# Performance work log

Hardware: AMD Instinct MI355X
Metric: run time of the kernel (lower is better)

The kernel has to match this reference:

```python
import jax, jax.numpy as jnp
import numpy as np

D_MODEL = 1024
NUM_HEADS = 16
HEAD_DIM = D_MODEL // NUM_HEADS


def setup_inputs() -> dict:
    key = jax.random.key(0)
    ks = jax.random.split(key, 9)
    s = D_MODEL ** -0.5  # roughly like nn.Linear init scale
    x = jax.random.normal(ks[0], (4, 2048, D_MODEL), dtype=jnp.float32)
    Wq = jax.random.normal(ks[1], (D_MODEL, D_MODEL), dtype=jnp.float32) * s
    bq = jax.random.normal(ks[2], (D_MODEL,), dtype=jnp.float32) * s
    Wk = jax.random.normal(ks[3], (D_MODEL, D_MODEL), dtype=jnp.float32) * s
    bk = jax.random.normal(ks[4], (D_MODEL,), dtype=jnp.float32) * s
    Wv = jax.random.normal(ks[5], (D_MODEL, D_MODEL), dtype=jnp.float32) * s
    bv = jax.random.normal(ks[6], (D_MODEL,), dtype=jnp.float32) * s
    Wo = jax.random.normal(ks[7], (D_MODEL, D_MODEL), dtype=jnp.float32) * s
    bo = jax.random.normal(ks[8], (D_MODEL,), dtype=jnp.float32) * s
    return {"x": x, "Wq": Wq, "bq": bq, "Wk": Wk, "bk": bk,
            "Wv": Wv, "bv": bv, "Wo": Wo, "bo": bo}


def reference(x, Wq, bq, Wk, bk, Wv, bv, Wo, bo):
    B, S, D = x.shape
    H, Dh = NUM_HEADS, HEAD_DIM
    scale = Dh ** -0.5
    # nn.Linear: x @ W.T + b
    q = (x @ Wq.T + bq).reshape(B, S, H, Dh)
    k = (x @ Wk.T + bk).reshape(B, S, H, Dh)
    v = (x @ Wv.T + bv).reshape(B, S, H, Dh)
    # scores: (B, H, S, S), full materialization as in the original bmm path
    dp = scale * jnp.einsum('bqhd,bkhd->bhqk', q, k)
    att = jax.nn.softmax(dp, axis=-1)
    out = jnp.einsum('bhqk,bkhd->bqhd', att, v).reshape(B, S, D)
    return out @ Wo.T + bo
```

## Files before the change

kernel.cpp:

```cpp
#include <hip/hip_runtime.h>
#include <stdint.h>

typedef __attribute__((ext_vector_type(8))) __bf16 bf16x8;
typedef __attribute__((ext_vector_type(4))) float floatx4;

#define DEV __device__ __forceinline__

DEV unsigned short f2bf(float f) {
    union { float f; unsigned u; } uf; uf.f = f;
    unsigned u = uf.u;
    unsigned r = (u + 0x7fffu + ((u >> 16) & 1u)) >> 16;
    return (unsigned short)r;
}

DEV float fast_exp2(float x) {
#if __has_builtin(__builtin_amdgcn_exp2f)
    return __builtin_amdgcn_exp2f(x);
#else
    return exp2f(x);
#endif
}

DEV unsigned pack_trunc2(float lo, float hi) {
    return __builtin_amdgcn_perm(__float_as_uint(hi), __float_as_uint(lo), 0x07060302u);
}

DEV void async16(const void* g, void* l) {
    __builtin_amdgcn_global_load_lds(
        (const __attribute__((address_space(1))) void*)g,
        (__attribute__((address_space(3))) void*)l, 16, 0, 0);
}

__global__ void cast_bf16_kernel(const float* __restrict__ src,
                                 unsigned short* __restrict__ dst, int n4) {
    int i = blockIdx.x * blockDim.x + threadIdx.x;
    if (i >= n4) return;
    float4 v = reinterpret_cast<const float4*>(src)[i];
    ushort4 o;
    o.x = f2bf(v.x); o.y = f2bf(v.y); o.z = f2bf(v.z); o.w = f2bf(v.w);
    reinterpret_cast<ushort4*>(dst)[i] = o;
}

__global__ void cast_w_kernel(const float* __restrict__ Wq, const float* __restrict__ Wk,
                              const float* __restrict__ Wv, const float* __restrict__ Wo,
                              const float* __restrict__ bq, const float* __restrict__ bk,
                              const float* __restrict__ bv,
                              unsigned short* __restrict__ wqkv,
                              unsigned short* __restrict__ wo,
                              float* __restrict__ bqkv) {
    const int NW = 262144;
    int i = blockIdx.x * blockDim.x + threadIdx.x;
    if (i < 4 * NW) {
        int seg = i >> 18, off = i & (NW - 1);
        const float* src = (seg == 0) ? Wq : (seg == 1) ? Wk : (seg == 2) ? Wv : Wo;
        unsigned short* dst = (seg < 3) ? (wqkv + seg * 1048576) : wo;
        float4 v = reinterpret_cast<const float4*>(src)[off];
        ushort4 o;
        o.x = f2bf(v.x); o.y = f2bf(v.y); o.z = f2bf(v.z); o.w = f2bf(v.w);
        reinterpret_cast<ushort4*>(dst)[off] = o;
    } else {
        int j = i - 4 * NW;
        if (j < 768) {
            int seg = j >> 8, off = j & 255;
            const float* src = (seg == 0) ? bq : (seg == 1) ? bk : bv;
            reinterpret_cast<float4*>(bqkv)[j] =
                reinterpret_cast<const float4*>(src)[off];
        }
    }
}

template <int MODE>
__global__ __launch_bounds__(256)
void gemm128(const unsigned short* __restrict__ A,
             const unsigned short* __restrict__ B,
             const float* __restrict__ bias,
             unsigned short* __restrict__ q_ws,
             unsigned short* __restrict__ k_ws,
             unsigned short* __restrict__ v_ws,
             float* __restrict__ fout) {
    constexpr int K = 1024;
    __shared__ alignas(16) unsigned short smem[128 * 136];
    unsigned short* sA = smem;
    unsigned short* sB = smem + 128 * 64;
    unsigned short* sT = smem;
    float* sT32 = reinterpret_cast<float*>(smem);

    const int tid = threadIdx.x;
    const int w = tid >> 6, lane = tid & 63, quad = lane >> 4, l16 = lane & 15;
    const int wr = w >> 1, wc = w & 1;
    const int bm = blockIdx.x, bn = blockIdx.y;
    const int arow0 = bm * 128, brow0 = bn * 128;

    floatx4 acc[4][4];
#pragma unroll
    for (int i = 0; i < 4; i++)
#pragma unroll
        for (int j = 0; j < 4; j++) acc[i][j] = (floatx4){0.f, 0.f, 0.f, 0.f};

    for (int k0 = 0; k0 < K; k0 += 64) {
#pragma unroll
        for (int i = 0; i < 4; i++) {
            int cb = i * 256 + w * 64;
            int ci = cb + lane;
            int row = ci >> 3, cl = ci & 7, cs = cl ^ (row & 7);
            async16(A + (size_t)(arow0 + row) * K + k0 + cs * 8, (char*)sA + cb * 16);
            async16(B + (size_t)(brow0 + row) * K + k0 + cs * 8, (char*)sB + cb * 16);
        }
        __syncthreads();
#pragma unroll
        for (int kk = 0; kk < 2; kk++) {
            bf16x8 aF[4], bF[4];
#pragma unroll
            for (int i = 0; i < 4; i++) {
                int row = wr * 64 + i * 16 + l16;
                int c = kk * 4 + quad, ph = c ^ (row & 7);
                aF[i] = *reinterpret_cast<const bf16x8*>(sA + row * 64 + ph * 8);
            }
#pragma unroll
            for (int j = 0; j < 4; j++) {
                int row = wc * 64 + j * 16 + l16;
                int c = kk * 4 + quad, ph = c ^ (row & 7);
                bF[j] = *reinterpret_cast<const bf16x8*>(sB + row * 64 + ph * 8);
            }
#pragma unroll
            for (int i = 0; i < 4; i++)
#pragma unroll
                for (int j = 0; j < 4; j++)
                    acc[i][j] = __builtin_amdgcn_mfma_f32_16x16x32_bf16(
                        aF[i], bF[j], acc[i][j], 0, 0, 0);
        }
        __syncthreads();
    }

    if (MODE == 1) {
#pragma unroll
        for (int ch = 0; ch < 2; ch++) {
            if (ch) __syncthreads();
            if (wr == ch) {
#pragma unroll
                for (int j = 0; j < 4; j++) {
                    const int c = wc * 64 + j * 16 + l16;
                    const float bia = bias[brow0 + c];
#pragma unroll
                    for (int i = 0; i < 4; i++) {
                        int s_loc = i * 16 + quad * 4;
#pragma unroll
                        for (int r = 0; r < 4; r++)
                            sT32[(s_loc + r) * 132 + c] = acc[i][j][r] + bia;
                    }
                }
            }
            __syncthreads();
            const int cpos = (tid & 31) * 4;
#pragma unroll
            for (int it = 0; it < 8; it++) {
                int s_loc = (tid >> 5) + it * 8;
                int grow = arow0 + ch * 64 + s_loc;
                float4 vv = *reinterpret_cast<const float4*>(sT32 + s_loc * 132 + cpos);
                *reinterpret_cast<float4*>(fout + (size_t)grow * 1024 + brow0 + cpos) = vv;
            }
        }
    } else if (bn < 16) {
        unsigned short* dst = (bn < 8) ? q_ws : k_ws;
        const float sc = (bn < 8) ? 0.18033688f : 1.0f;
#pragma unroll
        for (int j = 0; j < 4; j++) {
            const int c = wc * 64 + j * 16 + l16;
            const float bia = bias[brow0 + c];
#pragma unroll
            for (int i = 0; i < 4; i++) {
                int s_loc = wr * 64 + i * 16 + quad * 4;
#pragma unroll
                for (int r = 0; r < 4; r++)
                    sT[(s_loc + r) * 136 + c] = f2bf((acc[i][j][r] + bia) * sc);
            }
        }
        __syncthreads();
        const int nnbase = (bn & 7) * 128;
        const int c0 = (tid & 15) * 8;
        const int h = (nnbase + c0) >> 6, d = c0 & 63;
#pragma unroll
        for (int it = 0; it < 8; it++) {
            int s_loc = (tid >> 4) + it * 16;
            int s = arow0 + s_loc;
            int bb = s >> 11, s4 = s & 2047;
            uint4 vdat = *reinterpret_cast<const uint4*>(sT + s_loc * 136 + c0);
            *reinterpret_cast<uint4*>(
                dst + ((size_t)(bb * 16 + h) * 2048 + s4) * 64 + d) = vdat;
        }
    } else {
#pragma unroll
        for (int j = 0; j < 4; j++) {
            const int c = wc * 64 + j * 16 + l16;
            const float bia = bias[brow0 + c];
#pragma unroll
            for (int i = 0; i < 4; i++) {
                int v_hi = wr * 4 + i;
#pragma unroll
                for (int r = 0; r < 4; r++) {
                    int v = (quad * 4 + r) * 8 + v_hi;
                    sT[c * 136 + v] = f2bf(acc[i][j][r] + bia);
                }
            }
        }
        __syncthreads();
        const int bb = bm >> 4, blk = bm & 15;
        const int chunk = tid & 15;
#pragma unroll
        for (int it = 0; it < 8; it++) {
            int row = (tid >> 4) + it * 16;
            int h = (bn - 16) * 2 + (row >> 6), d = row & 63;
            ushort4 lo = *reinterpret_cast<const ushort4*>(sT + row * 136 + chunk * 8);
            ushort4 hi = *reinterpret_cast<const ushort4*>(sT + row * 136 + chunk * 8 + 4);
            size_t off = ((size_t)(bb * 16 + h) * 64 + d) * 2048 + blk * 128 + chunk * 8;
            *reinterpret_cast<ushort4*>(v_ws + off) = lo;
            *reinterpret_cast<ushort4*>(v_ws + off + 4) = hi;
        }
    }
}

__global__ __launch_bounds__(256, 5)
void attn_kernel(const unsigned short* __restrict__ q_ws,
                 const unsigned short* __restrict__ k_ws,
                 const unsigned short* __restrict__ v_ws,
                 unsigned short* __restrict__ o_ws) {
    __shared__ alignas(16) unsigned short smem[2 * 128 * 64];
    unsigned short* sK  = smem;
    unsigned short* sVt = smem + 128 * 64;

    const int tid = threadIdx.x;
    const int w = tid >> 6, lane = tid & 63, quad = lane >> 4, l16 = lane & 15;
    const int id = blockIdx.x;
    const int bh = (id >> 8) * 8 + (id & 7);
    const int q0 = ((id >> 3) & 31) * 64;
    const size_t base = (size_t)bh * 2048 * 64;

    unsigned short* sPw = smem + w * 2048;

    bf16x8 aQ[2];
    {
        int qrow = q0 + w * 16 + l16;
        const unsigned short* qp = q_ws + base + (size_t)qrow * 64 + quad * 8;
        aQ[0] = *reinterpret_cast<const bf16x8*>(qp);
        aQ[1] = *reinterpret_cast<const bf16x8*>(qp + 32);
    }

    const unsigned short* kptr[4];
    const unsigned short* vptr[4];
    char* klds[4];
    char* vlds[4];
#pragma unroll
    for (int i = 0; i < 4; i++) {
        int cb = i * 256 + w * 64;
        int ci = cb + lane;
        {
            int row = ci >> 3, cl = ci & 7, cs = cl ^ (row & 7);
            kptr[i] = k_ws + base + (size_t)row * 64 + cs * 8;
            klds[i] = (char*)sK + cb * 16;
        }
        {
            int row = ci >> 4, cl = ci & 15, cs = cl ^ (row & 15);
            vptr[i] = v_ws + base + (size_t)row * 2048 + cs * 8;
            vlds[i] = (char*)sVt + cb * 16;
        }
    }

    const __bf16 one = (__bf16)1.0f;
    const bf16x8 vOnes = {one, one, one, one, one, one, one, one};

    floatx4 oAcc[4], rsAcc;
#pragma unroll
    for (int j = 0; j < 4; j++) oAcc[j] = (floatx4){0.f, 0.f, 0.f, 0.f};
    rsAcc = (floatx4){0.f, 0.f, 0.f, 0.f};

    for (int t = 0; t < 16; t++) {
        const int kv0 = t * 128;
#pragma unroll
        for (int i = 0; i < 4; i++) {
            async16(kptr[i] + (size_t)kv0 * 64, klds[i]);
            async16(vptr[i] + kv0, vlds[i]);
        }
        __syncthreads();

        floatx4 sAcc[8];
#pragma unroll
        for (int j = 0; j < 8; j++) sAcc[j] = (floatx4){0.f, 0.f, 0.f, 0.f};
#pragma unroll
        for (int kk = 0; kk < 2; kk++) {
#pragma unroll
            for (int j = 0; j < 8; j++) {
                int krow = j * 16 + l16;
                int c = kk * 4 + quad, ph = c ^ (krow & 7);
                bf16x8 bK = *reinterpret_cast<const bf16x8*>(sK + krow * 64 + ph * 8);
                sAcc[j] = __builtin_amdgcn_mfma_f32_16x16x32_bf16(aQ[kk], bK, sAcc[j], 0, 0, 0);
            }
        }

        uint4 pk[4];
#pragma unroll
        for (int r = 0; r < 4; r++) {
            float e[8];
#pragma unroll
            for (int j = 0; j < 8; j++) e[j] = fast_exp2(sAcc[j][r]);
            pk[r].x = pack_trunc2(e[0], e[1]);
            pk[r].y = pack_trunc2(e[2], e[3]);
            pk[r].z = pack_trunc2(e[4], e[5]);
            pk[r].w = pack_trunc2(e[6], e[7]);
        }
        __syncthreads();

#pragma unroll
        for (int r = 0; r < 4; r++) {
            int row = quad * 4 + r;
            *reinterpret_cast<uint4*>(sPw + row * 128 + ((l16 ^ row) & 15) * 8) = pk[r];
        }
        asm volatile("s_waitcnt lgkmcnt(0)" ::: "memory");

        bf16x8 aP[4];
#pragma unroll
        for (int ks = 0; ks < 4; ks++)
            aP[ks] = *reinterpret_cast<const bf16x8*>(
                sPw + l16 * 128 + (((ks * 4 + quad) ^ l16) & 15) * 8);
#pragma unroll
        for (int jd = 0; jd < 4; jd++) {
            int drow = jd * 16 + l16;
#pragma unroll
            for (int ks = 0; ks < 4; ks++) {
                int c = ks * 4 + quad, ph = c ^ (drow & 15);
                bf16x8 bV = *reinterpret_cast<const bf16x8*>(sVt + drow * 128 + ph * 8);
                oAcc[jd] = __builtin_amdgcn_mfma_f32_16x16x32_bf16(aP[ks], bV, oAcc[jd], 0, 0, 0);
            }
        }
#pragma unroll
        for (int ks = 0; ks < 4; ks++)
            rsAcc = __builtin_amdgcn_mfma_f32_16x16x32_bf16(aP[ks], vOnes, rsAcc, 0, 0, 0);
        __syncthreads();
    }

    float inv[4];
#pragma unroll
    for (int r = 0; r < 4; r++) inv[r] = 1.0f / rsAcc[r];
    const int bb = bh >> 4, h = bh & 15;
#pragma unroll
    for (int jd = 0; jd < 4; jd++) {
        int d = jd * 16 + l16;
#pragma unroll
        for (int r = 0; r < 4; r++) {
            int s = q0 + w * 16 + quad * 4 + r;
            float v = oAcc[jd][r] * inv[r];
            o_ws[((size_t)bb * 2048 + s) * 1024 + h * 64 + d] = f2bf(v);
        }
    }
}

extern "C" void kernel_launch(void* const* d_in, const int* in_sizes, int n_in,
                              void* d_out, int out_size, void* d_ws, size_t ws_size,
                              hipStream_t stream) {
    const float* x  = (const float*)d_in[0];
    const float* Wq = (const float*)d_in[1];
    const float* bq = (const float*)d_in[2];
    const float* Wk = (const float*)d_in[3];
    const float* bk = (const float*)d_in[4];
    const float* Wv = (const float*)d_in[5];
    const float* bv = (const float*)d_in[6];
    const float* Wo = (const float*)d_in[7];
    const float* bo = (const float*)d_in[8];
    float* out = (float*)d_out;

    char* ws = (char*)d_ws;
    unsigned short* xb   = (unsigned short*)(ws);
    unsigned short* wqkv = (unsigned short*)(ws + (16ull << 20));
    unsigned short* wo   = (unsigned short*)(ws + (22ull << 20));
    float*          bqkv = (float*)(ws + (24ull << 20));
    unsigned short* q_ws = (unsigned short*)(ws + (25ull << 20));
    unsigned short* k_ws = (unsigned short*)(ws + (41ull << 20));
    unsigned short* v_ws = (unsigned short*)(ws + (57ull << 20));
    unsigned short* o_ws = xb;

    const int n4x = 8192 * 1024 / 4;
    cast_bf16_kernel<<<n4x / 256, 256, 0, stream>>>(x, xb, n4x);
    cast_w_kernel<<<4099, 256, 0, stream>>>(Wq, Wk, Wv, Wo, bq, bk, bv,
                                            wqkv, wo, bqkv);

    gemm128<0><<<dim3(64, 24), 256, 0, stream>>>(xb, wqkv, bqkv, q_ws, k_ws, v_ws, nullptr);
    attn_kernel<<<2048, 256, 0, stream>>>(q_ws, k_ws, v_ws, o_ws);
    gemm128<1><<<dim3(64, 8), 256, 0, stream>>>(o_ws, wo, bo, nullptr, nullptr, nullptr, out);
}
```

Baseline: 288.3 us.

## Double-buffer K/V tiles in attention and merge cast kernels

The attention kernel now walks the sequence in 64-key tiles and prefetches the next K/V tile into a second LDS buffer while computing on the current one. This leaves one barrier per iteration instead of three and lets global loads overlap with MFMA work. The x and weight cast kernels are merged into a single launch, and the V-transpose staging index in the QKV GEMM is remapped. The risk is higher LDS use and a lower occupancy hint (4 instead of 5), plus more loop iterations with smaller tiles.

```diff
diff --git a/kernel.cpp b/kernel.cpp
--- a/kernel.cpp
+++ b/kernel.cpp
@@ -31,41 +31,41 @@
         (__attribute__((address_space(3))) void*)l, 16, 0, 0);
 }
 
-__global__ void cast_bf16_kernel(const float* __restrict__ src,
-                                 unsigned short* __restrict__ dst, int n4) {
-    int i = blockIdx.x * blockDim.x + threadIdx.x;
-    if (i >= n4) return;
-    float4 v = reinterpret_cast<const float4*>(src)[i];
-    ushort4 o;
-    o.x = f2bf(v.x); o.y = f2bf(v.y); o.z = f2bf(v.z); o.w = f2bf(v.w);
-    reinterpret_cast<ushort4*>(dst)[i] = o;
-}
-
-__global__ void cast_w_kernel(const float* __restrict__ Wq, const float* __restrict__ Wk,
-                              const float* __restrict__ Wv, const float* __restrict__ Wo,
-                              const float* __restrict__ bq, const float* __restrict__ bk,
-                              const float* __restrict__ bv,
-                              unsigned short* __restrict__ wqkv,
-                              unsigned short* __restrict__ wo,
-                              float* __restrict__ bqkv) {
+__global__ void cast_all_kernel(const float* __restrict__ x,
+                                const float* __restrict__ Wq, const float* __restrict__ Wk,
+                                const float* __restrict__ Wv, const float* __restrict__ Wo,
+                                const float* __restrict__ bq, const float* __restrict__ bk,
+                                const float* __restrict__ bv,
+                                unsigned short* __restrict__ xb,
+                                unsigned short* __restrict__ wqkv,
+                                unsigned short* __restrict__ wo,
+                                float* __restrict__ bqkv) {
+    const int NX = 2097152;
     const int NW = 262144;
     int i = blockIdx.x * blockDim.x + threadIdx.x;
-    if (i < 4 * NW) {
-        int seg = i >> 18, off = i & (NW - 1);
+    if (i < NX) {
+        float4 v = reinterpret_cast<const float4*>(x)[i];
+        ushort4 o;
+        o.x = f2bf(v.x); o.y = f2bf(v.y); o.z = f2bf(v.z); o.w = f2bf(v.w);
+        reinterpret_cast<ushort4*>(xb)[i] = o;
+        return;
+    }
+    int j = i - NX;
+    if (j < 4 * NW) {
+        int seg = j >> 18, off = j & (NW - 1);
         const float* src = (seg == 0) ? Wq : (seg == 1) ? Wk : (seg == 2) ? Wv : Wo;
         unsigned short* dst = (seg < 3) ? (wqkv + seg * 1048576) : wo;
         float4 v = reinterpret_cast<const float4*>(src)[off];
         ushort4 o;
         o.x = f2bf(v.x); o.y = f2bf(v.y); o.z = f2bf(v.z); o.w = f2bf(v.w);
         reinterpret_cast<ushort4*>(dst)[off] = o;
-    } else {
-        int j = i - 4 * NW;
-        if (j < 768) {
-            int seg = j >> 8, off = j & 255;
-            const float* src = (seg == 0) ? bq : (seg == 1) ? bk : bv;
-            reinterpret_cast<float4*>(bqkv)[j] =
-                reinterpret_cast<const float4*>(src)[off];
-        }
+        return;
+    }
+    int k = j - 4 * NW;
+    if (k < 768) {
+        int seg = k >> 8, off = k & 255;
+        const float* src = (seg == 0) ? bq : (seg == 1) ? bk : bv;
+        reinterpret_cast<float4*>(bqkv)[k] = reinterpret_cast<const float4*>(src)[off];
     }
 }
 
@@ -195,10 +195,9 @@
             const float bia = bias[brow0 + c];
 #pragma unroll
             for (int i = 0; i < 4; i++) {
-                int v_hi = wr * 4 + i;
 #pragma unroll
                 for (int r = 0; r < 4; r++) {
-                    int v = (quad * 4 + r) * 8 + v_hi;
+                    int v = wr * 64 + (quad * 4 + r) * 4 + i;
                     sT[c * 136 + v] = f2bf(acc[i][j][r] + bia);
                 }
             }
@@ -219,14 +218,12 @@
     }
 }
 
-__global__ __launch_bounds__(256, 5)
+__global__ __launch_bounds__(256, 4)
 void attn_kernel(const unsigned short* __restrict__ q_ws,
                  const unsigned short* __restrict__ k_ws,
                  const unsigned short* __restrict__ v_ws,
                  unsigned short* __restrict__ o_ws) {
-    __shared__ alignas(16) unsigned short smem[2 * 128 * 64];
-    unsigned short* sK  = smem;
-    unsigned short* sVt = smem + 128 * 64;
+    __shared__ alignas(16) unsigned short smem[20480];
 
     const int tid = threadIdx.x;
     const int w = tid >> 6, lane = tid & 63, quad = lane >> 4, l16 = lane & 15;
@@ -235,7 +232,7 @@
     const int q0 = ((id >> 3) & 31) * 64;
     const size_t base = (size_t)bh * 2048 * 64;
 
-    unsigned short* sPw = smem + w * 2048;
+    unsigned short* sPw = smem + 16384 + w * 1024;
 
     bf16x8 aQ[2];
     {
@@ -245,24 +242,16 @@
         aQ[1] = *reinterpret_cast<const bf16x8*>(qp + 32);
     }
 
-    const unsigned short* kptr[4];
-    const unsigned short* vptr[4];
-    char* klds[4];
-    char* vlds[4];
-#pragma unroll
-    for (int i = 0; i < 4; i++) {
-        int cb = i * 256 + w * 64;
-        int ci = cb + lane;
-        {
-            int row = ci >> 3, cl = ci & 7, cs = cl ^ (row & 7);
-            kptr[i] = k_ws + base + (size_t)row * 64 + cs * 8;
-            klds[i] = (char*)sK + cb * 16;
-        }
-        {
-            int row = ci >> 4, cl = ci & 15, cs = cl ^ (row & 15);
-            vptr[i] = v_ws + base + (size_t)row * 2048 + cs * 8;
-            vlds[i] = (char*)sVt + cb * 16;
-        }
+    const unsigned short* kg[2];
+    const unsigned short* vg[2];
+    int loff[2];
+#pragma unroll
+    for (int it = 0; it < 2; it++) {
+        int ci = it * 256 + tid;
+        int row = ci >> 3, cl = ci & 7, cs = cl ^ (row & 7);
+        kg[it] = k_ws + base + (size_t)row * 64 + cs * 8;
+        vg[it] = v_ws + base + (size_t)row * 2048 + cs * 8;
+        loff[it] = ci * 8;
     }
 
     const __bf16 one = (__bf16)1.0f;
@@ -273,68 +262,78 @@
     for (int j = 0; j < 4; j++) oAcc[j] = (floatx4){0.f, 0.f, 0.f, 0.f};
     rsAcc = (floatx4){0.f, 0.f, 0.f, 0.f};
 
-    for (int t = 0; t < 16; t++) {
-        const int kv0 = t * 128;
-#pragma unroll
-        for (int i = 0; i < 4; i++) {
-            async16(kptr[i] + (size_t)kv0 * 64, klds[i]);
-            async16(vptr[i] + kv0, vlds[i]);
-        }
-        __syncthreads();
-
-        floatx4 sAcc[8];
-#pragma unroll
-        for (int j = 0; j < 8; j++) sAcc[j] = (floatx4){0.f, 0.f, 0.f, 0.f};
+    {
+#pragma unroll
+        for (int it = 0; it < 2; it++) {
+            async16(kg[it], smem + loff[it]);
+            async16(vg[it], smem + 8192 + loff[it]);
+        }
+    }
+
+    for (int t = 0; t < 32; t++) {
+        const int b = t & 1;
+        const unsigned short* sK = smem + b * 4096;
+        const unsigned short* sVt = smem + 8192 + b * 4096;
+        __syncthreads();
+
+        if (t < 31) {
+            const int kv0 = (t + 1) * 64;
+            unsigned short* dK = smem + (b ^ 1) * 4096;
+            unsigned short* dV = smem + 8192 + (b ^ 1) * 4096;
+#pragma unroll
+            for (int it = 0; it < 2; it++) {
+                async16(kg[it] + (size_t)kv0 * 64, dK + loff[it]);
+                async16(vg[it] + kv0, dV + loff[it]);
+            }
+        }
+
+        floatx4 sAcc[4];
+#pragma unroll
+        for (int j = 0; j < 4; j++) sAcc[j] = (floatx4){0.f, 0.f, 0.f, 0.f};
 #pragma unroll
         for (int kk = 0; kk < 2; kk++) {
 #pragma unroll
-            for (int j = 0; j < 8; j++) {
+            for (int j = 0; j < 4; j++) {
                 int krow = j * 16 + l16;
-                int c = kk * 4 + quad, ph = c ^ (krow & 7);
+                int ph = (kk * 4 + quad) ^ (krow & 7);
                 bf16x8 bK = *reinterpret_cast<const bf16x8*>(sK + krow * 64 + ph * 8);
                 sAcc[j] = __builtin_amdgcn_mfma_f32_16x16x32_bf16(aQ[kk], bK, sAcc[j], 0, 0, 0);
             }
         }
 
-        uint4 pk[4];
 #pragma unroll
         for (int r = 0; r < 4; r++) {
-            float e[8];
-#pragma unroll
-            for (int j = 0; j < 8; j++) e[j] = fast_exp2(sAcc[j][r]);
-            pk[r].x = pack_trunc2(e[0], e[1]);
-            pk[r].y = pack_trunc2(e[2], e[3]);
-            pk[r].z = pack_trunc2(e[4], e[5]);
-            pk[r].w = pack_trunc2(e[6], e[7]);
-        }
-        __syncthreads();
-
-#pragma unroll
-        for (int r = 0; r < 4; r++) {
-            int row = quad * 4 + r;
-            *reinterpret_cast<uint4*>(sPw + row * 128 + ((l16 ^ row) & 15) * 8) = pk[r];
+            float e0 = fast_exp2(sAcc[0][r]);
+            float e1 = fast_exp2(sAcc[1][r]);
+            float e2 = fast_exp2(sAcc[2][r]);
+            float e3 = fast_exp2(sAcc[3][r]);
+            uint2 pk;
+            pk.x = pack_trunc2(e0, e1);
+            pk.y = pack_trunc2(e2, e3);
+            int srow = quad * 4 + r;
+            int off = srow * 64 + (((l16 >> 1) ^ (srow & 7)) << 3) + (l16 & 1) * 4;
+            *reinterpret_cast<uint2*>(sPw + off) = pk;
         }
         asm volatile("s_waitcnt lgkmcnt(0)" ::: "memory");
 
-        bf16x8 aP[4];
-#pragma unroll
-        for (int ks = 0; ks < 4; ks++)
+        bf16x8 aP[2];
+#pragma unroll
+        for (int ks = 0; ks < 2; ks++)
             aP[ks] = *reinterpret_cast<const bf16x8*>(
-                sPw + l16 * 128 + (((ks * 4 + quad) ^ l16) & 15) * 8);
+                sPw + l16 * 64 + (((ks * 4 + quad) ^ (l16 & 7)) << 3));
 #pragma unroll
         for (int jd = 0; jd < 4; jd++) {
             int drow = jd * 16 + l16;
 #pragma unroll
-            for (int ks = 0; ks < 4; ks++) {
-                int c = ks * 4 + quad, ph = c ^ (drow & 15);
-                bf16x8 bV = *reinterpret_cast<const bf16x8*>(sVt + drow * 128 + ph * 8);
+            for (int ks = 0; ks < 2; ks++) {
+                int ph = (ks * 4 + quad) ^ (drow & 7);
+                bf16x8 bV = *reinterpret_cast<const bf16x8*>(sVt + drow * 64 + ph * 8);
                 oAcc[jd] = __builtin_amdgcn_mfma_f32_16x16x32_bf16(aP[ks], bV, oAcc[jd], 0, 0, 0);
             }
         }
 #pragma unroll
-        for (int ks = 0; ks < 4; ks++)
+        for (int ks = 0; ks < 2; ks++)
             rsAcc = __builtin_amdgcn_mfma_f32_16x16x32_bf16(aP[ks], vOnes, rsAcc, 0, 0, 0);
-        __syncthreads();
     }
 
     float inv[4];
@@ -377,10 +376,8 @@
     unsigned short* v_ws = (unsigned short*)(ws + (57ull << 20));
     unsigned short* o_ws = xb;
 
-    const int n4x = 8192 * 1024 / 4;
-    cast_bf16_kernel<<<n4x / 256, 256, 0, stream>>>(x, xb, n4x);
-    cast_w_kernel<<<4099, 256, 0, stream>>>(Wq, Wk, Wv, Wo, bq, bk, bv,
-                                            wqkv, wo, bqkv);
+    cast_all_kernel<<<12291, 256, 0, stream>>>(x, Wq, Wk, Wv, Wo, bq, bk, bv,
+                                               xb, wqkv, wo, bqkv);
 
     gemm128<0><<<dim3(64, 24), 256, 0, stream>>>(xb, wqkv, bqkv, q_ws, k_ws, v_ws, nullptr);
     attn_kernel<<<2048, 256, 0, stream>>>(q_ws, k_ws, v_ws, o_ws);
```

After: 283.1 us. No clear change (-1.8%).
